# Optimization experiments

Hardware: AMD Instinct MI355X
Metric: run time of the kernel (lower is better)

Reference implementation:

```python
import jax, jax.numpy as jnp
import numpy as np

# ---- dims (match init_kwargs / input_specs) ----
N = 50000        # nodes
E = 600000       # edges
F_IN = 128       # n_features
HID = 128        # hidden_dims
K = 8            # heads
D_A = 16         # attention dim per head
D_V = 16         # value dim per head
D_M = 64         # max-pool gate dim
CLASSES = 40     # n_classes
LAYERS = 2
SLOPE = 0.1      # negative_slop


def glorot(key, shape):
    lim = jnp.sqrt(6.0 / (shape[-2] + shape[-1]))
    return jax.random.uniform(key, shape, minval=-lim, maxval=lim, dtype=jnp.float32)


def setup_inputs() -> dict:
    key = jax.random.key(0)
    ks = jax.random.split(key, 10)
    x = jax.random.normal(ks[0], (N, F_IN), dtype=jnp.float32)
    edge_index = jax.random.randint(ks[1], (2, E), 0, N, dtype=jnp.int64)
    weight_in = glorot(ks[2], (F_IN, HID))
    weight_out = glorot(ks[3], (HID, CLASSES))
    # per-layer GaANConv params, stacked on leading layer dim
    Wq = glorot(ks[4], (LAYERS, HID, K * D_A))            # query proj
    Wk = glorot(ks[5], (LAYERS, HID, K * D_A))            # key proj
    Wv = glorot(ks[6], (LAYERS, HID, K * D_V))            # value proj
    Wm = glorot(ks[7], (LAYERS, HID, D_M))                # max-pool gate proj
    Wg = glorot(ks[8], (LAYERS, HID + D_M + HID, K))      # gate FC
    Wo = glorot(ks[9], (LAYERS, HID + K * D_V, HID))      # output proj
    return {"x": x, "edge_index": edge_index, "weight_in": weight_in,
            "weight_out": weight_out, "Wq": Wq, "Wk": Wk, "Wv": Wv,
            "Wm": Wm, "Wg": Wg, "Wo": Wo}


def gaan_conv(x, src, dst, wq, wk, wv, wm, wg, wo):
    n = x.shape[0]
    q = (x @ wq).reshape(n, K, D_A)
    k = (x @ wk).reshape(n, K, D_A)
    v = (x @ wv).reshape(n, K, D_V)
    # dot-product attention logits per edge/head: <q_dst, k_src>
    score = jnp.einsum('ekd,ekd->ek', q[dst], k[src])          # [E,K]
    # segment softmax over incoming edges of each dst node
    smax = jax.ops.segment_max(score, dst, num_segments=n)     # [N,K]
    smax = jnp.where(jnp.isfinite(smax), smax, 0.0)            # empty segments -> 0
    ex = jnp.exp(score - smax[dst])
    denom = jax.ops.segment_sum(ex, dst, num_segments=n)
    alpha = ex / (denom[dst] + 1e-16)                          # [E,K]
    agg = jax.ops.segment_sum(alpha[:, :, None] * v[src], dst, num_segments=n)  # [N,K,D_V]
    # gates: sigmoid(FC([x_i, max_j FC_m(x_j), mean_j x_j]))
    m = x @ wm                                                 # [N,D_M]
    maxpool = jax.ops.segment_max(m[src], dst, num_segments=n)
    maxpool = jnp.where(jnp.isfinite(maxpool), maxpool, 0.0)
    deg = jax.ops.segment_sum(jnp.ones((src.shape[0],), x.dtype), dst, num_segments=n)
    meanpool = jax.ops.segment_sum(x[src], dst, num_segments=n) / jnp.maximum(deg, 1.0)[:, None]
    g = jax.nn.sigmoid(jnp.concatenate([x, maxpool, meanpool], axis=1) @ wg)  # [N,K]
    gated = (g[:, :, None] * agg).reshape(n, K * D_V)
    return jnp.concatenate([x, gated], axis=1) @ wo            # [N,HID]


def reference(x, edge_index, weight_in, weight_out, Wq, Wk, Wv, Wm, Wg, Wo):
    src, dst = edge_index[0], edge_index[1]
    h = x @ weight_in
    for i in range(LAYERS):
        h = jax.nn.leaky_relu(
            gaan_conv(h, src, dst, Wq[i], Wk[i], Wv[i], Wm[i], Wg[i], Wo[i]),
            negative_slope=SLOPE)
        # dropout is identity in eval mode
    out = h @ weight_out
    return jax.nn.log_softmax(out, axis=1)
```

## Files before the change

### kernel.cpp

```cpp
#include <hip/hip_runtime.h>
#include <math.h>

#define NNODES 50000
#define NEDGES 600000
#define HIDDIM 128
#define NHEAD 8
#define DM 64
#define NCLS 40
#define FSTR 584
#define OFF_K 128
#define OFF_V 256
#define OFF_M 384
#define OFF_HG 448
#define OFF_H 456
#define NBLK 196

typedef __attribute__((ext_vector_type(8))) short short8;
typedef __attribute__((ext_vector_type(4))) float f32x4;

static __device__ __forceinline__ unsigned short f2bf(float f) {
    unsigned u = __float_as_uint(f);
    unsigned r = (u + 0x7fffu + ((u >> 16) & 1u)) >> 16;
    return (unsigned short)r;
}
static __device__ __forceinline__ float bflo(unsigned u) { return __uint_as_float(u << 16); }
static __device__ __forceinline__ float bfhi(unsigned u) { return __uint_as_float(u & 0xffff0000u); }
static __device__ __forceinline__ float bf2f(unsigned short s) {
    return __uint_as_float(((unsigned)s) << 16);
}

template <int WF32, int WB1, int ACT>
__global__ __launch_bounds__(256) void gemm_mfma(
    const unsigned short* __restrict__ A1, int lda1, int K1,
    const unsigned short* __restrict__ A2, int lda2, int K2,
    const unsigned short* __restrict__ BT,
    float* __restrict__ C, int ldc,
    unsigned short* __restrict__ Cb1, int ldb1, int off1,
    int M, int NN)
{
    const int K = K1 + K2;
    const int l = threadIdx.x & 63, wv = threadIdx.x >> 6;
    const int r = l & 15, g = l >> 4;
    const int row0 = blockIdx.y * 256 + wv * 64;
    const int col0 = blockIdx.x * 64;

    f32x4 acc[4][4] = {};

    for (int k0 = 0; k0 < K; k0 += 32) {
        const unsigned short* Ak;
        int ka, lda;
        if (k0 < K1) { Ak = A1; ka = k0; lda = lda1; }
        else         { Ak = A2; ka = k0 - K1; lda = lda2; }

        short8 a[4], b[4];
#pragma unroll
        for (int m = 0; m < 4; ++m) {
            int row = row0 + m * 16 + r;
            if (row < M)
                a[m] = *reinterpret_cast<const short8*>(Ak + (size_t)row * lda + ka + 8 * g);
            else
                a[m] = short8{0, 0, 0, 0, 0, 0, 0, 0};
        }
#pragma unroll
        for (int n = 0; n < 4; ++n) {
            int col = col0 + n * 16 + r;
            b[n] = *reinterpret_cast<const short8*>(BT + (size_t)col * K + k0 + 8 * g);
        }
#pragma unroll
        for (int m = 0; m < 4; ++m)
#pragma unroll
            for (int n = 0; n < 4; ++n)
                acc[m][n] = __builtin_amdgcn_mfma_f32_16x16x32_bf16(a[m], b[n], acc[m][n], 0, 0, 0);
    }

#pragma unroll
    for (int m = 0; m < 4; ++m) {
#pragma unroll
        for (int j = 0; j < 4; ++j) {
            int row = row0 + m * 16 + 4 * g + j;
            if (row >= M) continue;
#pragma unroll
            for (int n = 0; n < 4; ++n) {
                int col = col0 + n * 16 + r;
                if (col >= NN) continue;
                float vv = acc[m][n][j];
                if (ACT) vv = vv > 0.f ? vv : 0.1f * vv;
                if (WF32) C[(size_t)row * ldc + col] = vv;
                if (WB1)  Cb1[(size_t)row * ldb1 + off1 + col] = f2bf(vv);
            }
        }
    }
}

#define BT_TOTAL 206848
__global__ __launch_bounds__(256) void pack_weights(
    const float* __restrict__ w_in, const float* __restrict__ w_out,
    const float* __restrict__ Wq, const float* __restrict__ Wk,
    const float* __restrict__ Wv, const float* __restrict__ Wm,
    const float* __restrict__ Wg, const float* __restrict__ Wo,
    unsigned short* __restrict__ BT)
{
    int i = blockIdx.x * 256 + threadIdx.x;
    if (i >= BT_TOTAL) return;
    float val;
    if (i < 16384) {
        int c = i >> 7, k = i & 127;
        val = w_in[k * 128 + c];
    } else if (i < 133120) {
        int li = i - 16384;
        int L = li / 58368, t = li % 58368;
        int c = t >> 7, k = t & 127;
        if      (c < 128) val = Wq[L * 16384 + k * 128 + c];
        else if (c < 256) val = Wk[L * 16384 + k * 128 + (c - 128)];
        else if (c < 384) val = Wv[L * 16384 + k * 128 + (c - 256)];
        else if (c < 448) val = Wm[L * 8192  + k * 64  + (c - 384)];
        else              val = Wg[L * 2560 + (192 + k) * 8 + (c - 448)];
    } else if (i < 198656) {
        int li = i - 133120;
        int L = li / 32768, t = li % 32768;
        int c = t >> 8, k = t & 255;
        val = Wo[L * 32768 + k * 128 + c];
    } else {
        int t = i - 198656;
        int c = t >> 7, k = t & 127;
        val = (c < NCLS) ? w_out[k * NCLS + c] : 0.f;
    }
    BT[i] = f2bf(val);
}

__global__ __launch_bounds__(256) void convert_x_kernel(
    const float* __restrict__ x, unsigned int* __restrict__ xb2)
{
    int i = blockIdx.x * 256 + threadIdx.x;
    if (i >= NNODES * HIDDIM / 2) return;
    float2 f = *reinterpret_cast<const float2*>(x + (size_t)i * 2);
    xb2[i] = (unsigned)f2bf(f.x) | ((unsigned)f2bf(f.y) << 16);
}

__global__ __launch_bounds__(256) void hist_kernel(
    const int* __restrict__ ei, int* __restrict__ degi)
{
    int e = blockIdx.x * 256 + threadIdx.x;
    if (e >= NEDGES) return;
    unsigned d = (unsigned)ei[NEDGES + e]; if (d >= NNODES) d = 0;
    atomicAdd(&degi[d], 1);
}

static __device__ __forceinline__ int wave_incl_scan(int x, int lane) {
#pragma unroll
    for (int off = 1; off < 64; off <<= 1) {
        int n = __shfl_up(x, off);
        if (lane >= off) x += n;
    }
    return x;
}

__global__ __launch_bounds__(256) void scan_blk_kernel(
    const int* __restrict__ degi, int* __restrict__ rowptr,
    int* __restrict__ bsum)
{
    __shared__ int wsum[4];
    const int t = threadIdx.x, b = blockIdx.x;
    const int idx = b * 256 + t;
    const int lane = t & 63, wv = t >> 6;
    int v = (idx < NNODES) ? degi[idx] : 0;
    int incl = wave_incl_scan(v, lane);
    if (lane == 63) wsum[wv] = incl;
    __syncthreads();
    int wpre = 0;
#pragma unroll
    for (int w = 0; w < 4; ++w) wpre += (w < wv) ? wsum[w] : 0;
    if (idx < NNODES) rowptr[idx] = wpre + incl - v;
    if (t == 255) bsum[b] = wpre + incl;
}

__global__ __launch_bounds__(256) void scan_top_kernel(
    const int* __restrict__ bsum, int* __restrict__ boff,
    int* __restrict__ rowptr)
{
    __shared__ int wsum[4];
    const int t = threadIdx.x;
    const int lane = t & 63, wv = t >> 6;
    int v = (t < NBLK) ? bsum[t] : 0;
    int incl = wave_incl_scan(v, lane);
    if (lane == 63) wsum[wv] = incl;
    __syncthreads();
    int wpre = 0;
#pragma unroll
    for (int w = 0; w < 4; ++w) wpre += (w < wv) ? wsum[w] : 0;
    if (t < NBLK) boff[t] = wpre + incl - v;
    if (t == 0) rowptr[NNODES] = NEDGES;
}

__global__ __launch_bounds__(256) void scan_add_kernel(
    int* __restrict__ rowptr, const int* __restrict__ boff)
{
    int idx = blockIdx.x * 256 + threadIdx.x;
    if (idx < NNODES) rowptr[idx] += boff[blockIdx.x];
}

__global__ __launch_bounds__(256) void scatter_kernel(
    const int* __restrict__ ei, const int* __restrict__ rowptr,
    int* __restrict__ fill, int* __restrict__ csr_src)
{
    int e = blockIdx.x * 256 + threadIdx.x;
    if (e >= NEDGES) return;
    unsigned s = (unsigned)ei[e];          if (s >= NNODES) s = 0;
    unsigned d = (unsigned)ei[NEDGES + e]; if (d >= NNODES) d = 0;
    int pos = rowptr[d] + atomicAdd(&fill[d], 1);
    csr_src[pos] = (int)s;
}

__global__ __launch_bounds__(256) void fused_edge_kernel(
    const int* __restrict__ rowptr, const int* __restrict__ csr_src,
    const unsigned short* __restrict__ feat, const float* __restrict__ Wg,
    unsigned short* __restrict__ gatedb)
{
    int node = blockIdx.x * 4 + (threadIdx.x >> 6);
    if (node >= NNODES) return;
    const int lane = threadIdx.x & 63;
    const int c2 = lane * 2;
    const int j0 = lane & 7;

    const int start = rowptr[node], end = rowptr[node + 1];
    const int deg = end - start;

    const unsigned short* frow = feat + (size_t)node * FSTR;
    unsigned qu = *reinterpret_cast<const unsigned*>(frow + c2);
    float qx = bflo(qu), qy = bfhi(qu);

    float mr = -INFINITY, dr = 0.f;
    float a0 = 0.f, a1 = 0.f;
    float hgs = 0.f;
    float mm = -INFINITY;

    int p = start;
    for (; p + 2 <= end; p += 2) {
        int s0 = csr_src[p], s1 = csr_src[p + 1];
        const unsigned short* r0 = feat + (size_t)s0 * FSTR;
        const unsigned short* r1 = feat + (size_t)s1 * FSTR;
        unsigned ku0 = *reinterpret_cast<const unsigned*>(r0 + OFF_K + c2);
        unsigned vu0 = *reinterpret_cast<const unsigned*>(r0 + OFF_V + c2);
        float    mv0 = bf2f(r0[OFF_M + lane]);
        float    hg0 = bf2f(r0[OFF_HG + j0]);
        unsigned ku1 = *reinterpret_cast<const unsigned*>(r1 + OFF_K + c2);
        unsigned vu1 = *reinterpret_cast<const unsigned*>(r1 + OFF_V + c2);
        float    mv1 = bf2f(r1[OFF_M + lane]);
        float    hg1 = bf2f(r1[OFF_HG + j0]);

        float sc0 = qx * bflo(ku0) + qy * bfhi(ku0);
        float sc1 = qx * bflo(ku1) + qy * bfhi(ku1);
        sc0 += __shfl_xor(sc0, 1);  sc1 += __shfl_xor(sc1, 1);
        sc0 += __shfl_xor(sc0, 2);  sc1 += __shfl_xor(sc1, 2);
        sc0 += __shfl_xor(sc0, 4);  sc1 += __shfl_xor(sc1, 4);

        float nm = fmaxf(mr, fmaxf(sc0, sc1));
        float scale = __expf(mr - nm);
        float e0 = __expf(sc0 - nm), e1 = __expf(sc1 - nm);
        dr = dr * scale + e0 + e1;
        a0 = a0 * scale; a0 = fmaf(e0, bflo(vu0), a0); a0 = fmaf(e1, bflo(vu1), a0);
        a1 = a1 * scale; a1 = fmaf(e0, bfhi(vu0), a1); a1 = fmaf(e1, bfhi(vu1), a1);
        mr = nm;

        hgs += hg0 + hg1;
        mm = fmaxf(mm, fmaxf(mv0, mv1));
    }
    if (p < end) {
        int s0 = csr_src[p];
        const unsigned short* r0 = feat + (size_t)s0 * FSTR;
        unsigned ku0 = *reinterpret_cast<const unsigned*>(r0 + OFF_K + c2);
        unsigned vu0 = *reinterpret_cast<const unsigned*>(r0 + OFF_V + c2);
        float    mv0 = bf2f(r0[OFF_M + lane]);
        float    hg0 = bf2f(r0[OFF_HG + j0]);

        float sc0 = qx * bflo(ku0) + qy * bfhi(ku0);
        sc0 += __shfl_xor(sc0, 1);
        sc0 += __shfl_xor(sc0, 2);
        sc0 += __shfl_xor(sc0, 4);

        float nm = fmaxf(mr, sc0);
        float scale = __expf(mr - nm);
        float e0 = __expf(sc0 - nm);
        dr = dr * scale + e0;
        a0 = fmaf(e0, bflo(vu0), a0 * scale);
        a1 = fmaf(e0, bfhi(vu0), a1 * scale);
        mr = nm;

        hgs += hg0;
        mm = fmaxf(mm, mv0);
    }

    float inv  = 1.f / (dr + 1e-16f);
    float invd = 1.f / fmaxf((float)deg, 1.f);
    if (deg == 0) { mm = 0.f; inv = 0.f; }

    unsigned hou = *reinterpret_cast<const unsigned*>(frow + OFF_H + c2);
    float hx = bflo(hou), hy = bfhi(hou);

    const float* w0 = Wg + (size_t)c2 * 8;
    const float* w1 = Wg + (size_t)(c2 + 1) * 8;
    const float* w2 = Wg + (size_t)(128 + lane) * 8;

    float part[8];
#pragma unroll
    for (int j = 0; j < 8; ++j)
        part[j] = hx * w0[j] + hy * w1[j] + mm * w2[j];
#pragma unroll
    for (int off = 1; off < 64; off <<= 1)
#pragma unroll
        for (int j = 0; j < 8; ++j)
            part[j] += __shfl_xor(part[j], off);

    float mc = __shfl(hgs, lane >> 3);
    float gg = 1.f / (1.f + __expf(-(part[lane >> 3] + mc * invd)));
    float o0 = gg * a0 * inv, o1 = gg * a1 * inv;
    unsigned outu = (unsigned)f2bf(o0) | ((unsigned)f2bf(o1) << 16);
    *reinterpret_cast<unsigned*>(gatedb + (size_t)node * HIDDIM + c2) = outu;
}

__global__ __launch_bounds__(256) void logsoftmax_kernel(float* __restrict__ out)
{
    int gt = blockIdx.x * 256 + threadIdx.x;
    int wid = gt >> 6;
    int lane = threadIdx.x & 63;
    if (wid >= NNODES) return;
    float* row = out + (size_t)wid * NCLS;
    float x = (lane < NCLS) ? row[lane] : -INFINITY;
    float mx = x;
#pragma unroll
    for (int off = 32; off; off >>= 1) mx = fmaxf(mx, __shfl_xor(mx, off));
    float ex = (lane < NCLS) ? __expf(x - mx) : 0.f;
    float sm = ex;
#pragma unroll
    for (int off = 32; off; off >>= 1) sm += __shfl_xor(sm, off);
    float lse = mx + logf(sm);
    if (lane < NCLS) row[lane] = x - lse;
}

static inline int cdiv(int a, int b) { return (a + b - 1) / b; }

extern "C" void kernel_launch(void* const* d_in, const int* in_sizes, int n_in,
                              void* d_out, int out_size, void* d_ws, size_t ws_size,
                              hipStream_t stream)
{
    const float* x     = (const float*)d_in[0];
    const int*   ei    = (const int*)d_in[1];
    const float* w_in  = (const float*)d_in[2];
    const float* w_out = (const float*)d_in[3];
    const float* Wq    = (const float*)d_in[4];
    const float* Wk    = (const float*)d_in[5];
    const float* Wv    = (const float*)d_in[6];
    const float* Wm    = (const float*)d_in[7];
    const float* Wg    = (const float*)d_in[8];
    const float* Wo    = (const float*)d_in[9];
    float* out = (float*)d_out;

    const size_t NF = NNODES;
    unsigned short* xb     = (unsigned short*)d_ws;
    unsigned short* feat0  = xb    + NF * 128;
    unsigned short* feat1  = feat0 + NF * FSTR;
    unsigned short* gatedb = feat1 + NF * FSTR;
    unsigned short* BTpool = gatedb + NF * 128;
    int* rowptr  = (int*)(BTpool + BT_TOTAL);
    int* degi    = rowptr + (NNODES + 1);
    int* fill    = degi + NNODES;
    int* csr_src = fill + NNODES;
    int* bsum    = csr_src + NEDGES;
    int* boff    = bsum + NBLK;

    const unsigned short* BTin    = BTpool;
    const unsigned short* BTqkvm0 = BTpool + 16384;
    const unsigned short* BTqkvm1 = BTpool + 74752;
    const unsigned short* BTo0    = BTpool + 133120;
    const unsigned short* BTo1    = BTpool + 165888;
    const unsigned short* BTout   = BTpool + 198656;

    pack_weights<<<cdiv(BT_TOTAL, 256), 256, 0, stream>>>(
        w_in, w_out, Wq, Wk, Wv, Wm, Wg, Wo, BTpool);
    convert_x_kernel<<<cdiv(NNODES * HIDDIM / 2, 256), 256, 0, stream>>>(
        x, (unsigned int*)xb);
    hipMemsetAsync(degi, 0, 2 * NNODES * sizeof(int), stream);
    hist_kernel<<<cdiv(NEDGES, 256), 256, 0, stream>>>(ei, degi);
    scan_blk_kernel<<<NBLK, 256, 0, stream>>>(degi, rowptr, bsum);
    scan_top_kernel<<<1, 256, 0, stream>>>(bsum, boff, rowptr);
    scan_add_kernel<<<NBLK, 256, 0, stream>>>(rowptr, boff);
    scatter_kernel<<<cdiv(NEDGES, 256), 256, 0, stream>>>(ei, rowptr, fill, csr_src);

    const dim3 g128(2, cdiv(NNODES, 256));
    const dim3 g456(8, cdiv(NNODES, 256));
    const dim3 g40 (1, cdiv(NNODES, 256));

    gemm_mfma<0, 1, 0><<<g128, 256, 0, stream>>>(
        xb, 128, 128, nullptr, 0, 0, BTin,
        nullptr, 0, feat0, FSTR, OFF_H, NNODES, 128);

    unsigned short* featA = feat0;
    unsigned short* featB = feat1;
    for (int L = 0; L < 2; ++L) {
        const unsigned short* btq = L ? BTqkvm1 : BTqkvm0;
        const unsigned short* bto = L ? BTo1 : BTo0;
        const float* wg = Wg + (size_t)L * 320 * 8;

        gemm_mfma<0, 1, 0><<<g456, 256, 0, stream>>>(
            featA + OFF_H, FSTR, 128, nullptr, 0, 0, btq,
            nullptr, 0, featA, FSTR, 0, NNODES, 456);

        fused_edge_kernel<<<cdiv(NNODES, 4), 256, 0, stream>>>(
            rowptr, csr_src, featA, wg, gatedb);

        gemm_mfma<0, 1, 1><<<g128, 256, 0, stream>>>(
            featA + OFF_H, FSTR, 128, gatedb, 128, 128, bto,
            nullptr, 0, featB, FSTR, OFF_H, NNODES, 128);

        unsigned short* t = featA; featA = featB; featB = t;
    }

    gemm_mfma<1, 0, 0><<<g40, 256, 0, stream>>>(
        featA + OFF_H, FSTR, 128, nullptr, 0, 0, BTout,
        out, NCLS, nullptr, 0, 0, NNODES, NCLS);
    logsoftmax_kernel<<<cdiv(NNODES * 64, 256), 256, 0, stream>>>(out);
}
```

Measured before the change: 475.3 us.

## Keep A rows in registers and loop over all output column tiles

```diff
diff --git a/kernel.cpp b/kernel.cpp
--- a/kernel.cpp
+++ b/kernel.cpp
@@ -29,8 +29,8 @@
     return __uint_as_float(((unsigned)s) << 16);
 }
 
-template <int WF32, int WB1, int ACT>
-__global__ __launch_bounds__(256) void gemm_mfma(
+template <int KCHUNKS, int WF32, int WB1, int ACT>
+__global__ __launch_bounds__(256) void gemm_1p(
     const unsigned short* __restrict__ A1, int lda1, int K1,
     const unsigned short* __restrict__ A2, int lda2, int K2,
     const unsigned short* __restrict__ BT,
@@ -38,55 +38,65 @@
     unsigned short* __restrict__ Cb1, int ldb1, int off1,
     int M, int NN)
 {
-    const int K = K1 + K2;
+    const int K = KCHUNKS * 32;
     const int l = threadIdx.x & 63, wv = threadIdx.x >> 6;
     const int r = l & 15, g = l >> 4;
-    const int row0 = blockIdx.y * 256 + wv * 64;
-    const int col0 = blockIdx.x * 64;
-
-    f32x4 acc[4][4] = {};
-
-    for (int k0 = 0; k0 < K; k0 += 32) {
+    const int row0 = blockIdx.y * 128 + wv * 32;
+
+    short8 a[KCHUNKS][2];
+#pragma unroll
+    for (int kc = 0; kc < KCHUNKS; ++kc) {
+        int kg = kc * 32;
         const unsigned short* Ak;
         int ka, lda;
-        if (k0 < K1) { Ak = A1; ka = k0; lda = lda1; }
-        else         { Ak = A2; ka = k0 - K1; lda = lda2; }
-
-        short8 a[4], b[4];
-#pragma unroll
-        for (int m = 0; m < 4; ++m) {
+        if (kg < K1) { Ak = A1; ka = kg; lda = lda1; }
+        else         { Ak = A2; ka = kg - K1; lda = lda2; }
+#pragma unroll
+        for (int m = 0; m < 2; ++m) {
             int row = row0 + m * 16 + r;
             if (row < M)
-                a[m] = *reinterpret_cast<const short8*>(Ak + (size_t)row * lda + ka + 8 * g);
+                a[kc][m] = *reinterpret_cast<const short8*>(Ak + (size_t)row * lda + ka + 8 * g);
             else
-                a[m] = short8{0, 0, 0, 0, 0, 0, 0, 0};
+                a[kc][m] = short8{0, 0, 0, 0, 0, 0, 0, 0};
         }
-#pragma unroll
-        for (int n = 0; n < 4; ++n) {
-            int col = col0 + n * 16 + r;
-            b[n] = *reinterpret_cast<const short8*>(BT + (size_t)col * K + k0 + 8 * g);
-        }
-#pragma unroll
-        for (int m = 0; m < 4; ++m)
-#pragma unroll
-            for (int n = 0; n < 4; ++n)
-                acc[m][n] = __builtin_amdgcn_mfma_f32_16x16x32_bf16(a[m], b[n], acc[m][n], 0, 0, 0);
-    }
-
-#pragma unroll
-    for (int m = 0; m < 4; ++m) {
-#pragma unroll
-        for (int j = 0; j < 4; ++j) {
-            int row = row0 + m * 16 + 4 * g + j;
-            if (row >= M) continue;
+    }
+
+    const int ntiles = (NN + 63) >> 6;
+    for (int t = 0; t < ntiles; ++t) {
+        const int col0 = t * 64;
+        f32x4 acc[2][4] = {};
+#pragma unroll
+        for (int kc = 0; kc < KCHUNKS; ++kc) {
+            short8 b[4];
 #pragma unroll
             for (int n = 0; n < 4; ++n) {
                 int col = col0 + n * 16 + r;
-                if (col >= NN) continue;
-                float vv = acc[m][n][j];
-                if (ACT) vv = vv > 0.f ? vv : 0.1f * vv;
-                if (WF32) C[(size_t)row * ldc + col] = vv;
-                if (WB1)  Cb1[(size_t)row * ldb1 + off1 + col] = f2bf(vv);
+                if (col < NN)
+                    b[n] = *reinterpret_cast<const short8*>(BT + (size_t)col * K + kc * 32 + 8 * g);
+                else
+                    b[n] = short8{0, 0, 0, 0, 0, 0, 0, 0};
+            }
+#pragma unroll
+            for (int m = 0; m < 2; ++m)
+#pragma unroll
+                for (int n = 0; n < 4; ++n)
+                    acc[m][n] = __builtin_amdgcn_mfma_f32_16x16x32_bf16(a[kc][m], b[n], acc[m][n], 0, 0, 0);
+        }
+#pragma unroll
+        for (int m = 0; m < 2; ++m) {
+#pragma unroll
+            for (int j = 0; j < 4; ++j) {
+                int row = row0 + m * 16 + 4 * g + j;
+                if (row >= M) continue;
+#pragma unroll
+                for (int n = 0; n < 4; ++n) {
+                    int col = col0 + n * 16 + r;
+                    if (col >= NN) continue;
+                    float vv = acc[m][n][j];
+                    if (ACT) vv = vv > 0.f ? vv : 0.1f * vv;
+                    if (WF32) C[(size_t)row * ldc + col] = vv;
+                    if (WB1)  Cb1[(size_t)row * ldb1 + off1 + col] = f2bf(vv);
+                }
             }
         }
     }
@@ -386,11 +396,9 @@
     scan_add_kernel<<<NBLK, 256, 0, stream>>>(rowptr, boff);
     scatter_kernel<<<cdiv(NEDGES, 256), 256, 0, stream>>>(ei, rowptr, fill, csr_src);
 
-    const dim3 g128(2, cdiv(NNODES, 256));
-    const dim3 g456(8, cdiv(NNODES, 256));
-    const dim3 g40 (1, cdiv(NNODES, 256));
-
-    gemm_mfma<0, 1, 0><<<g128, 256, 0, stream>>>(
+    const dim3 gM(1, cdiv(NNODES, 128));
+
+    gemm_1p<4, 0, 1, 0><<<gM, 256, 0, stream>>>(
         xb, 128, 128, nullptr, 0, 0, BTin,
         nullptr, 0, feat0, FSTR, OFF_H, NNODES, 128);
 
@@ -401,21 +409,21 @@
         const unsigned short* bto = L ? BTo1 : BTo0;
         const float* wg = Wg + (size_t)L * 320 * 8;
 
-        gemm_mfma<0, 1, 0><<<g456, 256, 0, stream>>>(
+        gemm_1p<4, 0, 1, 0><<<gM, 256, 0, stream>>>(
             featA + OFF_H, FSTR, 128, nullptr, 0, 0, btq,
             nullptr, 0, featA, FSTR, 0, NNODES, 456);
 
         fused_edge_kernel<<<cdiv(NNODES, 4), 256, 0, stream>>>(
             rowptr, csr_src, featA, wg, gatedb);
 
-        gemm_mfma<0, 1, 1><<<g128, 256, 0, stream>>>(
+        gemm_1p<8, 0, 1, 1><<<gM, 256, 0, stream>>>(
             featA + OFF_H, FSTR, 128, gatedb, 128, 128, bto,
             nullptr, 0, featB, FSTR, OFF_H, NNODES, 128);
 
         unsigned short* t = featA; featA = featB; featB = t;
     }
 
-    gemm_mfma<1, 0, 0><<<g40, 256, 0, stream>>>(
+    gemm_1p<4, 1, 0, 0><<<gM, 256, 0, stream>>>(
         featA + OFF_H, FSTR, 128, nullptr, 0, 0, BTout,
         out, NCLS, nullptr, 0, 0, NNODES, NCLS);
     logsoftmax_kernel<<<cdiv(NNODES * 64, 256), 256, 0, stream>>>(out);
```

Result: faster. 465.4 us (-2.1%).
